# Performance work log

Hardware: AMD Instinct MI355X
Metric: run time of the kernel (lower is better)

Reference implementation:

```python
import jax, jax.numpy as jnp
import numpy as np
from jax import lax

S, T, B = 32, 32, 512          # src len, tgt len, batch
H, E, A = 1024, 256, 1024      # hidden, embed, attention dim
VS, VT = 64, 70                # source / target char vocab
START = 1                      # data.tar_l2i[start_token]


def _gru_cell(gi, h, W_hh, b_hh):
    """torch GRUCell math. gi = x @ W_ih.T + b_ih, shape (B, 3H)."""
    gh = h @ W_hh.T + b_hh
    ir, iz, in_ = jnp.split(gi, 3, axis=-1)
    hr, hz, hn = jnp.split(gh, 3, axis=-1)
    r = jax.nn.sigmoid(ir + hr)
    z = jax.nn.sigmoid(iz + hz)
    n = jnp.tanh(in_ + r * hn)
    return (1.0 - z) * n + z * h


def setup_inputs() -> dict:
    key = jax.random.key(0)
    ks = jax.random.split(key, 16)
    n = lambda k, shp: jax.random.normal(k, shp, dtype=jnp.float32) * 0.05
    return {
        "source": jax.random.randint(ks[0], (S, B), 0, VS),
        "target": jax.random.randint(ks[1], (T, B), 0, VT),
        "teacher_forcing": 1,
        "emb_src": n(ks[2], (VS, E)),
        "W_ih_enc": n(ks[3], (3 * H, E)),
        "W_hh_enc": n(ks[4], (3 * H, H)),
        "b_ih_enc": n(ks[5], (3 * H,)),
        "b_hh_enc": n(ks[6], (3 * H,)),
        "emb_tgt": n(ks[7], (VT, E)),
        "W_attn": n(ks[8], (2 * H, A)),
        "b_attn": n(ks[9], (A,)),
        "v_attn": n(ks[10], (A,)),
        "W_ih_dec": n(ks[11], (3 * H, H + E)),
        "W_hh_dec": n(ks[12], (3 * H, H)),
        "b_ih_dec": n(ks[13], (3 * H,)),
        "b_hh_dec": n(ks[14], (3 * H,)),
        "W_out": n(ks[15], (H, VT)),
        "b_out": jnp.zeros((VT,), jnp.float32),
    }


def reference(source, target, teacher_forcing, emb_src, W_ih_enc, W_hh_enc,
              b_ih_enc, b_hh_enc, emb_tgt, W_attn, b_attn, v_attn,
              W_ih_dec, W_hh_dec, b_ih_dec, b_hh_dec, W_out, b_out):
    tf = bool(teacher_forcing)

    # ---------------- Encoder: GRU over (S, B) ----------------
    x_emb = emb_src[source]                                   # (S, B, E)
    # precompute input-to-hidden GEMM for all timesteps (big fused GEMM)
    gi_all = jnp.einsum('sbe,ge->sbg', x_emb, W_ih_enc) + b_ih_enc  # (S, B, 3H)

    def enc_step(h, gi_t):
        h = _gru_cell(gi_t, h, W_hh_enc, b_hh_enc)
        return h, h

    h0 = jnp.zeros((B, H), x_emb.dtype)
    h_enc, enc_ops = lax.scan(enc_step, h0, gi_all)           # enc_ops: (S, B, H)

    # ---------------- Decoder loop (t = 1 .. T-1) ----------------
    def dec_step(carry, tgt_t):
        h, x = carry
        emb = emb_tgt[x]                                      # (B, E)
        hx = jnp.broadcast_to(h[None], (S, B, H))
        feat = jnp.concatenate([hx, enc_ops], axis=-1)        # (S, B, 2H)
        energy = jnp.tanh(jnp.einsum('sbf,fa->sba', feat, W_attn) + b_attn)
        scores = energy @ v_attn                              # (S, B)
        alpha = jax.nn.softmax(scores, axis=0)                # over source positions
        ctx = jnp.einsum('sb,sbh->bh', alpha, enc_ops)        # (B, H)
        gi = jnp.concatenate([ctx, emb], axis=-1) @ W_ih_dec.T + b_ih_dec
        h_new = _gru_cell(gi, h, W_hh_dec, b_hh_dec)
        logits = h_new @ W_out + b_out                        # (B, VT)
        x_next = tgt_t if tf else jnp.argmax(logits, axis=1)
        return (h_new, x_next), (logits, alpha.T)             # attn row: (B, S)

    (_, _), (dec_logits, attn) = lax.scan(dec_step, (h_enc, target[0]), target[1:])

    # outputs[0] is the one-hot start token (outputs[:, :, start]=1, rows 1.. overwritten)
    row0 = jnp.zeros((B, VT), dec_logits.dtype).at[:, START].set(1.0)
    outputs = jnp.concatenate([row0[None], dec_logits], axis=0)  # (T, B, VT)
    return outputs, attn                                         # attn: (T-1, B, S)
```

## Files before the change

kernel.cpp:

```cpp
#include <hip/hip_runtime.h>
#include <hip/hip_bf16.h>

typedef __bf16 bfx8 __attribute__((ext_vector_type(8)));
typedef __bf16 bfx4 __attribute__((ext_vector_type(4)));
typedef float f32x4 __attribute__((ext_vector_type(4)));

#define MFMA __builtin_amdgcn_mfma_f32_16x16x32_bf16


__device__ __attribute__((aligned(256))) float  g_h[512 * 1024];
__device__ __attribute__((aligned(256))) float  g_hpart[512 * 1024];
__device__ __attribute__((aligned(256))) __bf16 g_hb[2][512 * 1024];
__device__ __attribute__((aligned(256))) __bf16 g_Adec[512 * 1280];
__device__ __attribute__((aligned(256))) __bf16 g_enc_ops[(size_t)32 * 512 * 1024];
__device__ __attribute__((aligned(256))) __bf16 g_enc_part[(size_t)32 * 512 * 1024];
__device__ __attribute__((aligned(256))) __bf16 g_sWhhe[(size_t)3072 * 1024];
__device__ __attribute__((aligned(256))) __bf16 g_sWihe[(size_t)3072 * 256];
__device__ __attribute__((aligned(256))) __bf16 g_sWhhd[(size_t)3072 * 1024];
__device__ __attribute__((aligned(256))) __bf16 g_sWihd[(size_t)3072 * 1280];
__device__ __attribute__((aligned(256))) __bf16 g_sWattnA[(size_t)1024 * 1024];
__device__ __attribute__((aligned(256))) __bf16 g_sWattnB[(size_t)1024 * 1024];
__device__ __attribute__((aligned(256))) __bf16 g_sWout[(size_t)128 * 1024];
__device__ __attribute__((aligned(256))) __bf16 g_embs[64 * 256];
__device__ __attribute__((aligned(256))) __bf16 g_embt[70 * 256];

__device__ __forceinline__ float fast_tanh(float x) {
    float cx = fminf(fmaxf(x, -15.f), 15.f);
    float e = __expf(-2.f * cx);
    return (1.f - e) / (1.f + e);
}

__global__ void k_cvt(const float* __restrict__ src, __bf16* __restrict__ dst,
                      int n4)
{
    int i = blockIdx.x * 256 + threadIdx.x;
    if (i >= n4) return;
    float4 v = ((const float4*)src)[i];
    __bf16 o[4] = {(__bf16)v.x, (__bf16)v.y, (__bf16)v.z, (__bf16)v.w};
    *(ushort2*)(dst + 4 * i) = *(ushort2*)o;
    *(ushort2*)(dst + 4 * i + 2) = *(ushort2*)(o + 2);
}

__global__ void swz_rm(const float* __restrict__ W, __bf16* __restrict__ out,
                       int nK, int total)
{
    int gid = blockIdx.x * 256 + threadIdx.x;
    if (gid >= total) return;
    int F = gid >> 6, L = gid & 63;
    int t = F / nK, c = F - t * nK;
    int K = nK * 32;
    const float* s = W + (size_t)(t * 16 + (L & 15)) * K + c * 32 + (L >> 4) * 8;
    __bf16 o[8];
#pragma unroll
    for (int u = 0; u < 8; u++) o[u] = (__bf16)s[u];
    *(uint4*)(out + (size_t)gid * 8) = *(uint4*)o;
}

__global__ void swz_cm(const float* __restrict__ W, __bf16* __restrict__ out,
                       int nK, int ldsrc, int nguard, int total)
{
    int gid = blockIdx.x * 256 + threadIdx.x;
    if (gid >= total) return;
    int F = gid >> 6, L = gid & 63;
    int t = F / nK, c = F - t * nK;
    int n = t * 16 + (L & 15);
    int k = c * 32 + (L >> 4) * 8;
    __bf16 o[8];
#pragma unroll
    for (int u = 0; u < 8; u++)
        o[u] = (n < nguard) ? (__bf16)W[(size_t)(k + u) * ldsrc + n] : (__bf16)0.f;
    *(uint4*)(out + (size_t)gid * 8) = *(uint4*)o;
}

__global__ void k_init(float* __restrict__ out)
{
    int idx = blockIdx.x * 256 + threadIdx.x;
    if (idx < 512 * 1024) { g_h[idx] = 0.f; g_hb[0][idx] = (__bf16)0.f; }
    if (idx < 512 * 70) out[idx] = (idx % 70 == 1) ? 1.f : 0.f;
}

__global__ __launch_bounds__(512, 4) void k_encpart(
    const __bf16* __restrict__ Amat, const __bf16* __restrict__ sW,
    __bf16* __restrict__ Cout)
{
    __shared__ __bf16 sA[2][64 * 256];
    const int tid = threadIdx.x;
    const int w = tid >> 6, lane = tid & 63;
    const int r15 = lane & 15, q = lane >> 4;
    const int n0 = blockIdx.x * 256, m0 = blockIdx.y * 64;

    int sr[4], sv[4], so[4];
#pragma unroll
    for (int i = 0; i < 4; i++) {
        int lin = tid + i * 512;
        sr[i] = lin >> 5;
        sv[i] = lin & 31;
        so[i] = (sr[i] * 32 + (sv[i] ^ (sr[i] & 7))) * 8;
    }

    uint4 regs[4];
#pragma unroll
    for (int i = 0; i < 4; i++)
        regs[i] = *(const uint4*)(Amat + (size_t)(m0 + sr[i]) * 1024 + sv[i] * 8);
#pragma unroll
    for (int i = 0; i < 4; i++)
        *(uint4*)(&sA[0][so[i]]) = regs[i];
    __syncthreads();

    const int xk = r15 & 7;
    f32x4 acc[2][4];
#pragma unroll
    for (int nn = 0; nn < 2; nn++)
#pragma unroll
        for (int mf = 0; mf < 4; mf++) acc[nn][mf] = (f32x4){0.f, 0.f, 0.f, 0.f};

    const __bf16* wp0 = sW + ((size_t)(blockIdx.x * 16 + w * 2) * 32) * 512 + lane * 8;
    const __bf16* wp1 = wp0 + 32 * 512;
    const int ar0 = r15 * 256;
    const int ar1 = (16 + r15) * 256;
    const int ar2 = (32 + r15) * 256;
    const int ar3 = (48 + r15) * 256;

    for (int kc = 0; kc < 4; kc++) {
        if (kc < 3) {
#pragma unroll
            for (int i = 0; i < 4; i++)
                regs[i] = *(const uint4*)(Amat + (size_t)(m0 + sr[i]) * 1024 +
                                          (kc + 1) * 256 + sv[i] * 8);
        }
        const __bf16* sAb = sA[kc & 1];
        const __bf16* wq0 = wp0 + kc * 8 * 512;
        const __bf16* wq1 = wp1 + kc * 8 * 512;
#pragma unroll
        for (int c = 0; c < 8; c++) {
            int us = ((c * 4 + q) ^ xk) * 8;
            bfx8 a0 = *(const bfx8*)(sAb + ar0 + us);
            bfx8 a1 = *(const bfx8*)(sAb + ar1 + us);
            bfx8 a2 = *(const bfx8*)(sAb + ar2 + us);
            bfx8 a3 = *(const bfx8*)(sAb + ar3 + us);
            bfx8 w0 = *(const bfx8*)(wq0 + c * 512);
            bfx8 w1 = *(const bfx8*)(wq1 + c * 512);
            acc[0][0] = MFMA(a0, w0, acc[0][0], 0, 0, 0);
            acc[0][1] = MFMA(a1, w0, acc[0][1], 0, 0, 0);
            acc[0][2] = MFMA(a2, w0, acc[0][2], 0, 0, 0);
            acc[0][3] = MFMA(a3, w0, acc[0][3], 0, 0, 0);
            acc[1][0] = MFMA(a0, w1, acc[1][0], 0, 0, 0);
            acc[1][1] = MFMA(a1, w1, acc[1][1], 0, 0, 0);
            acc[1][2] = MFMA(a2, w1, acc[1][2], 0, 0, 0);
            acc[1][3] = MFMA(a3, w1, acc[1][3], 0, 0, 0);
        }
        if (kc < 3) {
#pragma unroll
            for (int i = 0; i < 4; i++)
                *(uint4*)(&sA[(kc + 1) & 1][so[i]]) = regs[i];
            __syncthreads();
        }
    }

#pragma unroll
    for (int nn = 0; nn < 2; nn++) {
        const int col = n0 + (w * 2 + nn) * 16 + r15;
#pragma unroll
        for (int mf = 0; mf < 4; mf++) {
#pragma unroll
            for (int reg = 0; reg < 4; reg++) {
                int row = m0 + mf * 16 + q * 4 + reg;
                Cout[(size_t)row * 1024 + col] = (__bf16)acc[nn][mf][reg];
            }
        }
    }
}

#define GH_BODY(ACC)                                              \
    {                                                             \
        int us = ((c * 4 + q) ^ xk) * 8;                          \
        bfx8 a0 = *(const bfx8*)(sA1 + br0 + us);                 \
        bfx8 a1 = *(const bfx8*)(sA1 + br1 + us);                 \
        bfx8 w0 = *(const bfx8*)(xp0 + c * 512);                  \
        bfx8 w1 = *(const bfx8*)(xp1 + c * 512);                  \
        bfx8 w2 = *(const bfx8*)(xp2 + c * 512);                  \
        ACC[0][0] = MFMA(a0, w0, ACC[0][0], 0, 0, 0);             \
        ACC[0][1] = MFMA(a1, w0, ACC[0][1], 0, 0, 0);             \
        ACC[1][0] = MFMA(a0, w1, ACC[1][0], 0, 0, 0);             \
        ACC[1][1] = MFMA(a1, w1, ACC[1][1], 0, 0, 0);             \
        ACC[2][0] = MFMA(a0, w2, ACC[2][0], 0, 0, 0);             \
        ACC[2][1] = MFMA(a1, w2, ACC[2][1], 0, 0, 0);             \
    }

__global__ __launch_bounds__(512, 1) void gru_step(
    const __bf16* __restrict__ hb_in, __bf16* __restrict__ hb_out,
    const __bf16* __restrict__ sW1, const float* __restrict__ b1,
    const __bf16* __restrict__ sW2, const float* __restrict__ b2,
    int nK2, const int* __restrict__ src_t, int enc_t)
{
    __shared__ __bf16 sA1[32 * 1024];
    __shared__ __bf16 sA2[32 * 1280];
    const int tid = threadIdx.x;
    const int w = tid >> 6, lane = tid & 63;
    const int r15 = lane & 15, q = lane >> 4;
    const int j0 = blockIdx.x * 64, m0 = blockIdx.y * 32;
    const int jsub = w & 3;

#pragma unroll
    for (int i = 0; i < 8; i++) {
        int lin = tid + i * 512;
        int r = lin >> 7, U = lin & 127;
        uint4 v = *(const uint4*)(hb_in + (size_t)(m0 + r) * 1024 + U * 8);
        *(uint4*)(sA1 + (r * 128 + (U ^ (r & 7))) * 8) = v;
    }
    if (src_t) {
#pragma unroll
        for (int i = 0; i < 2; i++) {
            int lin = tid + i * 512;
            int r = lin >> 5, U = lin & 31;
            int sv = src_t[m0 + r];
            sv = (sv < 0) ? 0 : (sv > 63 ? 63 : sv);
            uint4 v = *(const uint4*)(g_embs + sv * 256 + U * 8);
            *(uint4*)(sA2 + (r * 32 + (U ^ (r & 7))) * 8) = v;
        }
    } else {
        for (int lin = tid; lin < 32 * 160; lin += 512) {
            int r = lin / 160, U = lin - r * 160;
            uint4 v = *(const uint4*)(g_Adec + (size_t)(m0 + r) * 1280 + U * 8);
            *(uint4*)(sA2 + (r * 160 + (U ^ (r & 7))) * 8) = v;
        }
    }
    __syncthreads();

    const size_t tb = (size_t)(blockIdx.x * 4 + jsub);
    const int xk = r15 & 7;
    f32x4 acc[3][2];
#pragma unroll
    for (int s = 0; s < 3; s++)
#pragma unroll
        for (int ms = 0; ms < 2; ms++) acc[s][ms] = (f32x4){0.f, 0.f, 0.f, 0.f};

    if (w < 4) {
        const __bf16* xp0 = sW1 + (tb * 32) * 512 + lane * 8;
        const __bf16* xp1 = sW1 + ((tb + 64) * 32) * 512 + lane * 8;
        const __bf16* xp2 = sW1 + ((tb + 128) * 32) * 512 + lane * 8;
        const int br0 = r15 * 1024, br1 = (16 + r15) * 1024;
        if (src_t) {
#pragma unroll 4
            for (int c = 0; c < 20; c++) GH_BODY(acc)
        } else {
#pragma unroll 8
            for (int c = 0; c < 32; c++) GH_BODY(acc)
        }
    } else {
        const __bf16* wp0 = sW2 + (tb * (size_t)nK2) * 512 + lane * 8;
        const __bf16* wp1 = sW2 + ((tb + 64) * (size_t)nK2) * 512 + lane * 8;
        const __bf16* wp2 = sW2 + ((tb + 128) * (size_t)nK2) * 512 + lane * 8;
        const int ru = nK2 * 4;
        const int gr0 = r15 * ru * 8, gr1 = (16 + r15) * ru * 8;
#pragma unroll 8
        for (int c = 0; c < nK2; c++) {
            int us = ((c * 4 + q) ^ xk) * 8;
            bfx8 a0 = *(const bfx8*)(sA2 + gr0 + us);
            bfx8 a1 = *(const bfx8*)(sA2 + gr1 + us);
            bfx8 w0 = *(const bfx8*)(wp0 + c * 512);
            bfx8 w1 = *(const bfx8*)(wp1 + c * 512);
            bfx8 w2 = *(const bfx8*)(wp2 + c * 512);
            acc[0][0] = MFMA(a0, w0, acc[0][0], 0, 0, 0);
            acc[0][1] = MFMA(a1, w0, acc[0][1], 0, 0, 0);
            acc[1][0] = MFMA(a0, w1, acc[1][0], 0, 0, 0);
            acc[1][1] = MFMA(a1, w1, acc[1][1], 0, 0, 0);
            acc[2][0] = MFMA(a0, w2, acc[2][0], 0, 0, 0);
            acc[2][1] = MFMA(a1, w2, acc[2][1], 0, 0, 0);
        }
        if (src_t) {
            f32x4 acc2[3][2];
#pragma unroll
            for (int s = 0; s < 3; s++)
#pragma unroll
                for (int ms = 0; ms < 2; ms++) acc2[s][ms] = (f32x4){0.f, 0.f, 0.f, 0.f};
            const __bf16* xp0 = sW1 + (tb * 32) * 512 + lane * 8;
            const __bf16* xp1 = sW1 + ((tb + 64) * 32) * 512 + lane * 8;
            const __bf16* xp2 = sW1 + ((tb + 128) * 32) * 512 + lane * 8;
            const int br0 = r15 * 1024, br1 = (16 + r15) * 1024;
#pragma unroll 4
            for (int c = 20; c < 32; c++) GH_BODY(acc2)
            float* sGh = (float*)sA2 + 6144;
#pragma unroll
            for (int s = 0; s < 3; s++)
#pragma unroll
                for (int ms = 0; ms < 2; ms++)
#pragma unroll
                    for (int reg = 0; reg < 4; reg++)
                        sGh[((s * 4 + jsub) * 32 + ms * 16 + q * 4 + reg) * 16 + r15] =
                            acc2[s][ms][reg];
        }
    }
    __syncthreads();
    float* sGi = (float*)sA2;
    if (w >= 4) {
#pragma unroll
        for (int s = 0; s < 3; s++)
#pragma unroll
            for (int ms = 0; ms < 2; ms++)
#pragma unroll
                for (int reg = 0; reg < 4; reg++)
                    sGi[((s * 4 + jsub) * 32 + ms * 16 + q * 4 + reg) * 16 + r15] =
                        acc[s][ms][reg];
    }
    __syncthreads();
    if (w < 4) {
        const int jj = j0 + jsub * 16 + r15;
        const float bb1[3] = {b1[jj], b1[1024 + jj], b1[2048 + jj]};
        const float bb2[3] = {b2[jj], b2[1024 + jj], b2[2048 + jj]};
        const float* sGh = (const float*)sA2 + 6144;
#pragma unroll
        for (int ms = 0; ms < 2; ms++) {
#pragma unroll
            for (int reg = 0; reg < 4; reg++) {
                int bl = ms * 16 + q * 4 + reg;
                int b_ = m0 + bl;
                float e0 = 0.f, e1 = 0.f, e2 = 0.f;
                if (src_t) {
                    e0 = sGh[((0 * 4 + jsub) * 32 + bl) * 16 + r15];
                    e1 = sGh[((1 * 4 + jsub) * 32 + bl) * 16 + r15];
                    e2 = sGh[((2 * 4 + jsub) * 32 + bl) * 16 + r15];
                }
                float gh0 = acc[0][ms][reg] + bb1[0] + e0;
                float gh1 = acc[1][ms][reg] + bb1[1] + e1;
                float gh2 = acc[2][ms][reg] + bb1[2] + e2;
                float gi0 = sGi[((0 * 4 + jsub) * 32 + bl) * 16 + r15] + bb2[0];
                float gi1 = sGi[((1 * 4 + jsub) * 32 + bl) * 16 + r15] + bb2[1];
                float gi2 = sGi[((2 * 4 + jsub) * 32 + bl) * 16 + r15] + bb2[2];
                float r = 1.f / (1.f + __expf(-(gi0 + gh0)));
                float z = 1.f / (1.f + __expf(-(gi1 + gh1)));
                float n = fast_tanh(gi2 + r * gh2);
                size_t off = (size_t)b_ * 1024 + jj;
                float hv = (1.f - z) * n + z * g_h[off];
                g_h[off] = hv;
                hb_out[off] = (__bf16)hv;
                if (enc_t >= 0)
                    g_enc_ops[(size_t)enc_t * 524288 + off] = (__bf16)hv;
            }
        }
    }
}

__global__ __launch_bounds__(256) void k_hl(
    const __bf16* __restrict__ src, const float* __restrict__ battn,
    const float* __restrict__ bout, int lrow, float* __restrict__ outp)
{
    __shared__ __bf16 sA[32 * 1024];
    const int tid = threadIdx.x;
    const int w = tid >> 6, lane = tid & 63;
    const int r15 = lane & 15, q = lane >> 4;
    const int bx = blockIdx.x, m0 = blockIdx.y * 32;

#pragma unroll
    for (int i = 0; i < 16; i++) {
        int lin = tid + i * 256;
        int r = lin >> 7, U = lin & 127;
        uint4 v = *(const uint4*)(src + (size_t)(m0 + r) * 1024 + U * 8);
        *(uint4*)(sA + (r * 128 + (U ^ (r & 7))) * 8) = v;
    }
    __syncthreads();

    const __bf16* sW;
    int n;
    if (bx < 16) {
        sW = g_sWattnA;
        n = bx * 64 + w * 16 + r15;
    } else {
        if (lrow < 0) return;
        sW = g_sWout;
        n = (bx - 16) * 64 + w * 16 + r15;
    }
    const size_t tb = (size_t)((bx < 16 ? bx : bx - 16) * 4 + w);
    const __bf16* wp = sW + (tb * 32) * 512 + lane * 8;
    const int xk = r15 & 7;
    const int ar0 = r15 * 1024, ar1 = (16 + r15) * 1024;

    f32x4 acc[2];
    acc[0] = (f32x4){0.f, 0.f, 0.f, 0.f};
    acc[1] = (f32x4){0.f, 0.f, 0.f, 0.f};
#pragma unroll 8
    for (int c = 0; c < 32; c++) {
        int us = ((c * 4 + q) ^ xk) * 8;
        bfx8 a0 = *(const bfx8*)(sA + ar0 + us);
        bfx8 a1 = *(const bfx8*)(sA + ar1 + us);
        bfx8 wv = *(const bfx8*)(wp + c * 512);
        acc[0] = MFMA(a0, wv, acc[0], 0, 0, 0);
        acc[1] = MFMA(a1, wv, acc[1], 0, 0, 0);
    }

    if (bx < 16) {
        float bv = battn[n];
#pragma unroll
        for (int ms = 0; ms < 2; ms++)
#pragma unroll
            for (int reg = 0; reg < 4; reg++)
                g_hpart[(size_t)(m0 + ms * 16 + q * 4 + reg) * 1024 + n] =
                    acc[ms][reg] + bv;
    } else if (n < 70) {
        float bv = bout[n];
#pragma unroll
        for (int ms = 0; ms < 2; ms++)
#pragma unroll
            for (int reg = 0; reg < 4; reg++)
                outp[(size_t)lrow * 35840 +
                     (size_t)(m0 + ms * 16 + q * 4 + reg) * 70 + n] =
                    acc[ms][reg] + bv;
    }
}

__global__ __launch_bounds__(256) void k_attn(
    int j, const int* __restrict__ target, const int* __restrict__ tf,
    const float* __restrict__ v_attn, float* __restrict__ out)
{
    const int b = blockIdx.x, tid = threadIdx.x;
    const int lane = tid & 63, wave = tid >> 6;
    __shared__ float sc[32], sal[32];
    __shared__ int sx;
    if (wave == 0) {
        int xv;
        if (j == 0) xv = target[b];
        else if (*tf) xv = target[j * 512 + b];
        else {
            const float* row = out + (size_t)j * 35840 + b * 70;
            float bv = row[lane]; int bi = lane;
            if (lane < 6) {
                float v2 = row[lane + 64];
                if (v2 > bv) { bv = v2; bi = lane + 64; }
            }
#pragma unroll
            for (int off = 32; off; off >>= 1) {
                float ov = __shfl_down(bv, off);
                int   oi = __shfl_down(bi, off);
                if (ov > bv || (ov == bv && oi < bi)) { bv = ov; bi = oi; }
            }
            xv = bi;
        }
        if (lane == 0) sx = (xv < 0) ? 0 : (xv > 69 ? 69 : xv);
    }
    float hpv[16], vsv[16];
    {
        const float* hp = g_hpart + (size_t)b * 1024;
#pragma unroll
        for (int u = 0; u < 8; u++) {
            hpv[u]     = hp[lane * 8 + u];
            hpv[8 + u] = hp[512 + lane * 8 + u];
            vsv[u]     = v_attn[lane * 8 + u];
            vsv[8 + u] = v_attn[512 + lane * 8 + u];
        }
    }
    __syncthreads();
    g_Adec[(size_t)b * 1280 + 1024 + tid] = g_embt[sx * 256 + tid];
    for (int s = wave * 8; s < wave * 8 + 8; s++) {
        const __bf16* ep = g_enc_part + ((size_t)s * 512 + b) * 1024;
        bfx8 e0 = *(const bfx8*)(ep + lane * 8);
        bfx8 e1 = *(const bfx8*)(ep + 512 + lane * 8);
        float part = 0.f;
#pragma unroll
        for (int u = 0; u < 8; u++) {
            part += vsv[u]     * fast_tanh((float)e0[u] + hpv[u]);
            part += vsv[8 + u] * fast_tanh((float)e1[u] + hpv[8 + u]);
        }
#pragma unroll
        for (int off = 32; off; off >>= 1) part += __shfl_down(part, off);
        if (lane == 0) sc[s] = part;
    }
    __syncthreads();
    float mx = sc[0];
#pragma unroll
    for (int s = 1; s < 32; s++) mx = fmaxf(mx, sc[s]);
    float den = 0.f;
#pragma unroll
    for (int s = 0; s < 32; s++) den += __expf(sc[s] - mx);
    float rden = 1.f / den;
    if (tid < 32) {
        float al = __expf(sc[tid] - mx) * rden;
        sal[tid] = al;
        out[1146880 + (size_t)j * 16384 + b * 32 + tid] = al;
    }
    __syncthreads();
    float c0 = 0, c1 = 0, c2 = 0, c3 = 0;
    const __bf16* eo = g_enc_ops + (size_t)b * 1024 + tid * 4;
#pragma unroll 4
    for (int s = 0; s < 32; s++) {
        bfx4 e = *(const bfx4*)(eo + (size_t)s * 524288);
        float al = sal[s];
        c0 += al * (float)e[0]; c1 += al * (float)e[1];
        c2 += al * (float)e[2]; c3 += al * (float)e[3];
    }
    bfx4 o = {(__bf16)c0, (__bf16)c1, (__bf16)c2, (__bf16)c3};
    *(bfx4*)(&g_Adec[(size_t)b * 1280 + tid * 4]) = o;
}

extern "C" void kernel_launch(void* const* d_in, const int* in_sizes, int n_in,
                              void* d_out, int out_size, void* d_ws, size_t ws_size,
                              hipStream_t stream)
{
    const int*   source   = (const int*)d_in[0];
    const int*   target   = (const int*)d_in[1];
    const int*   tf       = (const int*)d_in[2];
    const float* emb_src  = (const float*)d_in[3];
    const float* W_ih_enc = (const float*)d_in[4];
    const float* W_hh_enc = (const float*)d_in[5];
    const float* b_ih_enc = (const float*)d_in[6];
    const float* b_hh_enc = (const float*)d_in[7];
    const float* emb_tgt  = (const float*)d_in[8];
    const float* W_attn   = (const float*)d_in[9];
    const float* b_attn   = (const float*)d_in[10];
    const float* v_attn   = (const float*)d_in[11];
    const float* W_ih_dec = (const float*)d_in[12];
    const float* W_hh_dec = (const float*)d_in[13];
    const float* b_ih_dec = (const float*)d_in[14];
    const float* b_hh_dec = (const float*)d_in[15];
    const float* W_out    = (const float*)d_in[16];
    const float* b_out    = (const float*)d_in[17];
    float* out = (float*)d_out;

    void *p_hb, *p_sWhhe, *p_sWihe, *p_sWhhd, *p_sWihd, *p_sWattnA, *p_sWattnB,
         *p_sWout, *p_embs, *p_embt, *p_enc_ops, *p_enc_part;
    hipGetSymbolAddress(&p_hb,       HIP_SYMBOL(g_hb));
    hipGetSymbolAddress(&p_sWhhe,    HIP_SYMBOL(g_sWhhe));
    hipGetSymbolAddress(&p_sWihe,    HIP_SYMBOL(g_sWihe));
    hipGetSymbolAddress(&p_sWhhd,    HIP_SYMBOL(g_sWhhd));
    hipGetSymbolAddress(&p_sWihd,    HIP_SYMBOL(g_sWihd));
    hipGetSymbolAddress(&p_sWattnA,  HIP_SYMBOL(g_sWattnA));
    hipGetSymbolAddress(&p_sWattnB,  HIP_SYMBOL(g_sWattnB));
    hipGetSymbolAddress(&p_sWout,    HIP_SYMBOL(g_sWout));
    hipGetSymbolAddress(&p_embs,     HIP_SYMBOL(g_embs));
    hipGetSymbolAddress(&p_embt,     HIP_SYMBOL(g_embt));
    hipGetSymbolAddress(&p_enc_ops,  HIP_SYMBOL(g_enc_ops));
    hipGetSymbolAddress(&p_enc_part, HIP_SYMBOL(g_enc_part));
    __bf16* hb0 = (__bf16*)p_hb;
    __bf16* hb1 = hb0 + 512 * 1024;

    k_cvt<<<16, 256, 0, stream>>>(emb_src, (__bf16*)p_embs, 64 * 256 / 4);
    k_cvt<<<18, 256, 0, stream>>>(emb_tgt, (__bf16*)p_embt, 70 * 256 / 4);
    swz_rm<<<1536, 256, 0, stream>>>(W_hh_enc, (__bf16*)p_sWhhe, 32, 393216);
    swz_rm<<<384,  256, 0, stream>>>(W_ih_enc, (__bf16*)p_sWihe, 8,  98304);
    swz_rm<<<1536, 256, 0, stream>>>(W_hh_dec, (__bf16*)p_sWhhd, 32, 393216);
    swz_rm<<<1920, 256, 0, stream>>>(W_ih_dec, (__bf16*)p_sWihd, 40, 491520);
    swz_cm<<<512,  256, 0, stream>>>(W_attn, (__bf16*)p_sWattnA, 32, 1024, 1024, 131072);
    swz_cm<<<512,  256, 0, stream>>>(W_attn + (size_t)1024 * 1024,
                                     (__bf16*)p_sWattnB, 32, 1024, 1024, 131072);
    swz_cm<<<64,   256, 0, stream>>>(W_out,  (__bf16*)p_sWout,   32, 70,   70,   16384);
    k_init<<<2048, 256, 0, stream>>>(out);

    for (int t = 0; t < 32; t++) {
        __bf16* hin  = (t & 1) ? hb1 : hb0;
        __bf16* hout = (t & 1) ? hb0 : hb1;
        gru_step<<<dim3(16, 16), 512, 0, stream>>>(
            hin, hout, (__bf16*)p_sWhhe, b_hh_enc,
            (__bf16*)p_sWihe, b_ih_enc, 8, source + t * 512, t);
    }

    k_encpart<<<dim3(4, 256), 512, 0, stream>>>(
        (__bf16*)p_enc_ops, (__bf16*)p_sWattnB, (__bf16*)p_enc_part);

    k_hl<<<dim3(18, 16), 256, 0, stream>>>(hb0, b_attn, b_out, -1, out);

    for (int j = 0; j < 31; j++) {
        __bf16* hin  = (j & 1) ? hb1 : hb0;
        __bf16* hout = (j & 1) ? hb0 : hb1;
        k_attn<<<512, 256, 0, stream>>>(j, target, tf, v_attn, out);
        gru_step<<<dim3(16, 16), 512, 0, stream>>>(
            hin, hout, (__bf16*)p_sWhhd, b_hh_dec,
            (__bf16*)p_sWihd, b_ih_dec, 40, nullptr, -1);
        k_hl<<<dim3(18, 16), 256, 0, stream>>>(hout, b_attn, b_out, j + 1, out);
    }
}
```

Baseline: 2.550 ms.

## Fuse encoder and decoder step loops into persistent cooperative kernels with grid sync

Replaces the per-timestep kernel launches (32 encoder GRU steps, and 31×3 decoder attention/GRU/projection launches) with two persistent cooperative kernels of 256 blocks that loop over timesteps and separate phases with grid-wide barriers. The attention and projection phases are remapped so that each 512-thread block handles two 256-thread sub-tasks, sharing one large dynamic-style shared buffer. The encoder-projection GEMM grid is flattened and swizzled so that neighbouring blocks reuse weight tiles. The aim is to remove launch overhead and inter-kernel gaps, at the cost of grid.sync latency, a requirement that all 256 blocks be co-resident (one per CU), and shared-memory sizing that limits occupancy.

```diff
diff --git a/kernel.cpp b/kernel.cpp
--- a/kernel.cpp
+++ b/kernel.cpp
@@ -1,5 +1,8 @@
 #include <hip/hip_runtime.h>
 #include <hip/hip_bf16.h>
+#include <hip/hip_cooperative_groups.h>
+
+namespace cg = cooperative_groups;
 
 typedef __bf16 bfx8 __attribute__((ext_vector_type(8)));
 typedef __bf16 bfx4 __attribute__((ext_vector_type(4)));
@@ -87,7 +90,9 @@
     const int tid = threadIdx.x;
     const int w = tid >> 6, lane = tid & 63;
     const int r15 = lane & 15, q = lane >> 4;
-    const int n0 = blockIdx.x * 256, m0 = blockIdx.y * 64;
+    const int sw = (blockIdx.x & 7) * 128 + (blockIdx.x >> 3);
+    const int nx = sw & 3;
+    const int n0 = nx * 256, m0 = (sw >> 2) * 64;
 
     int sr[4], sv[4], so[4];
 #pragma unroll
@@ -114,7 +119,7 @@
 #pragma unroll
         for (int mf = 0; mf < 4; mf++) acc[nn][mf] = (f32x4){0.f, 0.f, 0.f, 0.f};
 
-    const __bf16* wp0 = sW + ((size_t)(blockIdx.x * 16 + w * 2) * 32) * 512 + lane * 8;
+    const __bf16* wp0 = sW + ((size_t)(nx * 16 + w * 2) * 32) * 512 + lane * 8;
     const __bf16* wp1 = wp0 + 32 * 512;
     const int ar0 = r15 * 256;
     const int ar1 = (16 + r15) * 256;
@@ -187,18 +192,18 @@
         ACC[2][1] = MFMA(a1, w2, ACC[2][1], 0, 0, 0);             \
     }
 
-__global__ __launch_bounds__(512, 1) void gru_step(
-    const __bf16* __restrict__ hb_in, __bf16* __restrict__ hb_out,
-    const __bf16* __restrict__ sW1, const float* __restrict__ b1,
-    const __bf16* __restrict__ sW2, const float* __restrict__ b2,
-    int nK2, const int* __restrict__ src_t, int enc_t)
-{
-    __shared__ __bf16 sA1[32 * 1024];
-    __shared__ __bf16 sA2[32 * 1280];
+__device__ __forceinline__ void gru_phase(
+    unsigned char* smem_, const __bf16* hb_in, __bf16* hb_out,
+    const __bf16* sW1, const float* b1,
+    const __bf16* sW2, const float* b2,
+    int nK2, const int* src_t, int enc_t, int bid)
+{
+    __bf16* sA1 = (__bf16*)smem_;
+    __bf16* sA2 = (__bf16*)(smem_ + 65536);
     const int tid = threadIdx.x;
     const int w = tid >> 6, lane = tid & 63;
     const int r15 = lane & 15, q = lane >> 4;
-    const int j0 = blockIdx.x * 64, m0 = blockIdx.y * 32;
+    const int j0 = (bid & 15) * 64, m0 = (bid >> 4) * 32;
     const int jsub = w & 3;
 
 #pragma unroll
@@ -227,7 +232,7 @@
     }
     __syncthreads();
 
-    const size_t tb = (size_t)(blockIdx.x * 4 + jsub);
+    const size_t tb = (size_t)((bid & 15) * 4 + jsub);
     const int xk = r15 & 7;
     f32x4 acc[3][2];
 #pragma unroll
@@ -341,24 +346,32 @@
     }
 }
 
-__global__ __launch_bounds__(256) void k_hl(
-    const __bf16* __restrict__ src, const float* __restrict__ battn,
-    const float* __restrict__ bout, int lrow, float* __restrict__ outp)
-{
-    __shared__ __bf16 sA[32 * 1024];
+__device__ __forceinline__ void hl_phase(
+    unsigned char* smem_, const __bf16* src, const float* battn,
+    const float* bout, int lrow, float* outp, int bid)
+{
     const int tid = threadIdx.x;
-    const int w = tid >> 6, lane = tid & 63;
+    const int half = tid >> 8, t2 = tid & 255;
+    __bf16* sA = (__bf16*)(smem_ + half * 65536);
+    const int vb = bid + 256 * half;
+    const int active = vb < 288;
+    int bx = 0, m0 = 0;
+    if (active) { bx = vb % 18; m0 = (vb / 18) * 32; }
+    const int w = t2 >> 6, lane = tid & 63;
     const int r15 = lane & 15, q = lane >> 4;
-    const int bx = blockIdx.x, m0 = blockIdx.y * 32;
-
-#pragma unroll
-    for (int i = 0; i < 16; i++) {
-        int lin = tid + i * 256;
-        int r = lin >> 7, U = lin & 127;
-        uint4 v = *(const uint4*)(src + (size_t)(m0 + r) * 1024 + U * 8);
-        *(uint4*)(sA + (r * 128 + (U ^ (r & 7))) * 8) = v;
-    }
-    __syncthreads();
+    const int comp = active && !(bx >= 16 && lrow < 0);
+
+    if (comp) {
+#pragma unroll
+        for (int i = 0; i < 16; i++) {
+            int lin = t2 + i * 256;
+            int r = lin >> 7, U = lin & 127;
+            uint4 v = *(const uint4*)(src + (size_t)(m0 + r) * 1024 + U * 8);
+            *(uint4*)(sA + (r * 128 + (U ^ (r & 7))) * 8) = v;
+        }
+    }
+    __syncthreads();
+    if (!comp) return;
 
     const __bf16* sW;
     int n;
@@ -366,7 +379,6 @@
         sW = g_sWattnA;
         n = bx * 64 + w * 16 + r15;
     } else {
-        if (lrow < 0) return;
         sW = g_sWout;
         n = (bx - 16) * 64 + w * 16 + r15;
     }
@@ -408,15 +420,19 @@
     }
 }
 
-__global__ __launch_bounds__(256) void k_attn(
-    int j, const int* __restrict__ target, const int* __restrict__ tf,
-    const float* __restrict__ v_attn, float* __restrict__ out)
-{
-    const int b = blockIdx.x, tid = threadIdx.x;
-    const int lane = tid & 63, wave = tid >> 6;
-    __shared__ float sc[32], sal[32];
-    __shared__ int sx;
-    if (wave == 0) {
+__device__ __forceinline__ void attn_phase(
+    unsigned char* smem_, int j, const int* target, const int* tf,
+    const float* v_attn, float* out, int bid)
+{
+    const int tid = threadIdx.x;
+    const int half = tid >> 8, t2 = tid & 255;
+    const int b = bid * 2 + half;
+    const int lane = tid & 63, wave2 = t2 >> 6;
+    float* scH  = (float*)smem_ + half * 32;
+    float* salH = (float*)smem_ + 64 + half * 32;
+    int*   sxH  = (int*)(smem_ + 512) + half;
+
+    if (wave2 == 0) {
         int xv;
         if (j == 0) xv = target[b];
         else if (*tf) xv = target[j * 512 + b];
@@ -435,7 +451,7 @@
             }
             xv = bi;
         }
-        if (lane == 0) sx = (xv < 0) ? 0 : (xv > 69 ? 69 : xv);
+        if (lane == 0) *sxH = (xv < 0) ? 0 : (xv > 69 ? 69 : xv);
     }
     float hpv[16], vsv[16];
     {
@@ -449,8 +465,9 @@
         }
     }
     __syncthreads();
-    g_Adec[(size_t)b * 1280 + 1024 + tid] = g_embt[sx * 256 + tid];
-    for (int s = wave * 8; s < wave * 8 + 8; s++) {
+    int sx = *sxH;
+    g_Adec[(size_t)b * 1280 + 1024 + t2] = g_embt[sx * 256 + t2];
+    for (int s = wave2 * 8; s < wave2 * 8 + 8; s++) {
         const __bf16* ep = g_enc_part + ((size_t)s * 512 + b) * 1024;
         bfx8 e0 = *(const bfx8*)(ep + lane * 8);
         bfx8 e1 = *(const bfx8*)(ep + 512 + lane * 8);
@@ -462,33 +479,78 @@
         }
 #pragma unroll
         for (int off = 32; off; off >>= 1) part += __shfl_down(part, off);
-        if (lane == 0) sc[s] = part;
-    }
-    __syncthreads();
-    float mx = sc[0];
-#pragma unroll
-    for (int s = 1; s < 32; s++) mx = fmaxf(mx, sc[s]);
+        if (lane == 0) scH[s] = part;
+    }
+    __syncthreads();
+    float mx = scH[0];
+#pragma unroll
+    for (int s = 1; s < 32; s++) mx = fmaxf(mx, scH[s]);
     float den = 0.f;
 #pragma unroll
-    for (int s = 0; s < 32; s++) den += __expf(sc[s] - mx);
+    for (int s = 0; s < 32; s++) den += __expf(scH[s] - mx);
     float rden = 1.f / den;
-    if (tid < 32) {
-        float al = __expf(sc[tid] - mx) * rden;
-        sal[tid] = al;
-        out[1146880 + (size_t)j * 16384 + b * 32 + tid] = al;
+    if (t2 < 32) {
+        float al = __expf(scH[t2] - mx) * rden;
+        salH[t2] = al;
+        out[1146880 + (size_t)j * 16384 + b * 32 + t2] = al;
     }
     __syncthreads();
     float c0 = 0, c1 = 0, c2 = 0, c3 = 0;
-    const __bf16* eo = g_enc_ops + (size_t)b * 1024 + tid * 4;
+    const __bf16* eo = g_enc_ops + (size_t)b * 1024 + t2 * 4;
 #pragma unroll 4
     for (int s = 0; s < 32; s++) {
         bfx4 e = *(const bfx4*)(eo + (size_t)s * 524288);
-        float al = sal[s];
+        float al = salH[s];
         c0 += al * (float)e[0]; c1 += al * (float)e[1];
         c2 += al * (float)e[2]; c3 += al * (float)e[3];
     }
     bfx4 o = {(__bf16)c0, (__bf16)c1, (__bf16)c2, (__bf16)c3};
-    *(bfx4*)(&g_Adec[(size_t)b * 1280 + tid * 4]) = o;
+    *(bfx4*)(&g_Adec[(size_t)b * 1280 + t2 * 4]) = o;
+}
+
+__global__ void __launch_bounds__(512, 1) enc_all(
+    const int* __restrict__ source, const float* __restrict__ b1,
+    const float* __restrict__ b2, __bf16* __restrict__ hb0,
+    __bf16* __restrict__ hb1)
+{
+    __shared__ __align__(16) unsigned char smem[147456];
+    cg::grid_group grid = cg::this_grid();
+    const int bid = blockIdx.x;
+    __bf16* ha = hb0;
+    __bf16* hb = hb1;
+    for (int t = 0; t < 32; t++) {
+        if (t) grid.sync();
+        gru_phase(smem, ha, hb, g_sWhhe, b1, g_sWihe, b2, 8,
+                  source + t * 512, t, bid);
+        __bf16* tmp = ha; ha = hb; hb = tmp;
+    }
+}
+
+__global__ void __launch_bounds__(512, 1) dec_all(
+    const int* __restrict__ target, const int* __restrict__ tf,
+    const float* __restrict__ v_attn, const float* __restrict__ battn,
+    const float* __restrict__ bout, const float* __restrict__ b1,
+    const float* __restrict__ b2, float* __restrict__ out,
+    __bf16* __restrict__ hb0, __bf16* __restrict__ hb1)
+{
+    __shared__ __align__(16) unsigned char smem[147456];
+    cg::grid_group grid = cg::this_grid();
+    const int bid = blockIdx.x;
+
+    hl_phase(smem, hb0, battn, bout, -1, out, bid);
+    grid.sync();
+
+    __bf16* ha = hb0;
+    __bf16* hb = hb1;
+    for (int j = 0; j < 31; j++) {
+        attn_phase(smem, j, target, tf, v_attn, out, bid);
+        grid.sync();
+        gru_phase(smem, ha, hb, g_sWhhd, b1, g_sWihd, b2, 40, nullptr, -1, bid);
+        grid.sync();
+        hl_phase(smem, hb, battn, bout, j + 1, out, bid);
+        if (j < 30) grid.sync();
+        __bf16* tmp = ha; ha = hb; hb = tmp;
+    }
 }
 
 extern "C" void kernel_launch(void* const* d_in, const int* in_sizes, int n_in,
@@ -544,26 +606,21 @@
     swz_cm<<<64,   256, 0, stream>>>(W_out,  (__bf16*)p_sWout,   32, 70,   70,   16384);
     k_init<<<2048, 256, 0, stream>>>(out);
 
-    for (int t = 0; t < 32; t++) {
-        __bf16* hin  = (t & 1) ? hb1 : hb0;
-        __bf16* hout = (t & 1) ? hb0 : hb1;
-        gru_step<<<dim3(16, 16), 512, 0, stream>>>(
-            hin, hout, (__bf16*)p_sWhhe, b_hh_enc,
-            (__bf16*)p_sWihe, b_ih_enc, 8, source + t * 512, t);
-    }
-
-    k_encpart<<<dim3(4, 256), 512, 0, stream>>>(
+    {
+        void* args[] = {(void*)&source, (void*)&b_hh_enc, (void*)&b_ih_enc,
+                        (void*)&hb0, (void*)&hb1};
+        hipLaunchCooperativeKernel((const void*)enc_all, dim3(256), dim3(512),
+                                   args, 0, stream);
+    }
+
+    k_encpart<<<dim3(1024), 512, 0, stream>>>(
         (__bf16*)p_enc_ops, (__bf16*)p_sWattnB, (__bf16*)p_enc_part);
 
-    k_hl<<<dim3(18, 16), 256, 0, stream>>>(hb0, b_attn, b_out, -1, out);
-
-    for (int j = 0; j < 31; j++) {
-        __bf16* hin  = (j & 1) ? hb1 : hb0;
-        __bf16* hout = (j & 1) ? hb0 : hb1;
-        k_attn<<<512, 256, 0, stream>>>(j, target, tf, v_attn, out);
-        gru_step<<<dim3(16, 16), 512, 0, stream>>>(
-            hin, hout, (__bf16*)p_sWhhd, b_hh_dec,
-            (__bf16*)p_sWihd, b_ih_dec, 40, nullptr, -1);
-        k_hl<<<dim3(18, 16), 256, 0, stream>>>(hout, b_attn, b_out, j + 1, out);
-    }
-}
+    {
+        void* args[] = {(void*)&target, (void*)&tf, (void*)&v_attn,
+                        (void*)&b_attn, (void*)&b_out, (void*)&b_hh_dec,
+                        (void*)&b_ih_dec, (void*)&out, (void*)&hb0, (void*)&hb1};
+        hipLaunchCooperativeKernel((const void*)dec_all, dim3(256), dim3(512),
+                                   args, 0, stream);
+    }
+}
```

Result: slower. 6.755 ms (+164.9%).

## Split GRU step into smaller 256-thread blocks and remap encoder-part grid

Applied to the files above, without the earlier changes.

The GRU step kernel now runs 256-thread blocks covering 32 hidden columns each, with twice as many blocks and two blocks allowed per CU, to raise occupancy. The input-side operands (embeddings or the decoder input row) are read straight from global memory instead of being staged in shared memory, and the work is rebalanced so the hidden-side waves also take a slice of the decoder input GEMM. The encoder-part GEMM grid is flattened and remapped with a swizzled block order to improve cache locality. Reading operands directly from global memory trades shared-memory reuse for fewer barriers and less LDS use, and may cost extra global traffic.

```diff
diff --git a/kernel.cpp b/kernel.cpp
--- a/kernel.cpp
+++ b/kernel.cpp
@@ -87,7 +87,9 @@
     const int tid = threadIdx.x;
     const int w = tid >> 6, lane = tid & 63;
     const int r15 = lane & 15, q = lane >> 4;
-    const int n0 = blockIdx.x * 256, m0 = blockIdx.y * 64;
+    const int sw = (blockIdx.x & 7) * 128 + (blockIdx.x >> 3);
+    const int nx = sw & 3;
+    const int n0 = nx * 256, m0 = (sw >> 2) * 64;
 
     int sr[4], sv[4], so[4];
 #pragma unroll
@@ -114,7 +116,7 @@
 #pragma unroll
         for (int mf = 0; mf < 4; mf++) acc[nn][mf] = (f32x4){0.f, 0.f, 0.f, 0.f};
 
-    const __bf16* wp0 = sW + ((size_t)(blockIdx.x * 16 + w * 2) * 32) * 512 + lane * 8;
+    const __bf16* wp0 = sW + ((size_t)(nx * 16 + w * 2) * 32) * 512 + lane * 8;
     const __bf16* wp1 = wp0 + 32 * 512;
     const int ar0 = r15 * 256;
     const int ar1 = (16 + r15) * 256;
@@ -187,55 +189,58 @@
         ACC[2][1] = MFMA(a1, w2, ACC[2][1], 0, 0, 0);             \
     }
 
-__global__ __launch_bounds__(512, 1) void gru_step(
+#define GI_BODY(ACC)                                              \
+    {                                                             \
+        bfx8 a0 = *(const bfx8*)(A0 + c * 32);                    \
+        bfx8 a1 = *(const bfx8*)(A1 + c * 32);                    \
+        bfx8 w0 = *(const bfx8*)(wp0 + c * 512);                  \
+        bfx8 w1 = *(const bfx8*)(wp1 + c * 512);                  \
+        bfx8 w2 = *(const bfx8*)(wp2 + c * 512);                  \
+        ACC[0][0] = MFMA(a0, w0, ACC[0][0], 0, 0, 0);             \
+        ACC[0][1] = MFMA(a1, w0, ACC[0][1], 0, 0, 0);             \
+        ACC[1][0] = MFMA(a0, w1, ACC[1][0], 0, 0, 0);             \
+        ACC[1][1] = MFMA(a1, w1, ACC[1][1], 0, 0, 0);             \
+        ACC[2][0] = MFMA(a0, w2, ACC[2][0], 0, 0, 0);             \
+        ACC[2][1] = MFMA(a1, w2, ACC[2][1], 0, 0, 0);             \
+    }
+
+__global__ __launch_bounds__(256, 2) void gru_step(
     const __bf16* __restrict__ hb_in, __bf16* __restrict__ hb_out,
     const __bf16* __restrict__ sW1, const float* __restrict__ b1,
     const __bf16* __restrict__ sW2, const float* __restrict__ b2,
     int nK2, const int* __restrict__ src_t, int enc_t)
 {
-    __shared__ __bf16 sA1[32 * 1024];
-    __shared__ __bf16 sA2[32 * 1280];
+    __shared__ __align__(16) unsigned char smem[77824];
+    __bf16* sA1 = (__bf16*)smem;
+    float*  sGi = (float*)smem;
+    float*  sGh = (float*)(smem + 65536);
     const int tid = threadIdx.x;
     const int w = tid >> 6, lane = tid & 63;
     const int r15 = lane & 15, q = lane >> 4;
-    const int j0 = blockIdx.x * 64, m0 = blockIdx.y * 32;
-    const int jsub = w & 3;
-
-#pragma unroll
-    for (int i = 0; i < 8; i++) {
-        int lin = tid + i * 512;
+    const int j0 = blockIdx.x * 32, m0 = blockIdx.y * 32;
+    const int jsub = w & 1;
+
+#pragma unroll
+    for (int i = 0; i < 16; i++) {
+        int lin = tid + i * 256;
         int r = lin >> 7, U = lin & 127;
         uint4 v = *(const uint4*)(hb_in + (size_t)(m0 + r) * 1024 + U * 8);
         *(uint4*)(sA1 + (r * 128 + (U ^ (r & 7))) * 8) = v;
     }
-    if (src_t) {
-#pragma unroll
-        for (int i = 0; i < 2; i++) {
-            int lin = tid + i * 512;
-            int r = lin >> 5, U = lin & 31;
-            int sv = src_t[m0 + r];
-            sv = (sv < 0) ? 0 : (sv > 63 ? 63 : sv);
-            uint4 v = *(const uint4*)(g_embs + sv * 256 + U * 8);
-            *(uint4*)(sA2 + (r * 32 + (U ^ (r & 7))) * 8) = v;
-        }
-    } else {
-        for (int lin = tid; lin < 32 * 160; lin += 512) {
-            int r = lin / 160, U = lin - r * 160;
-            uint4 v = *(const uint4*)(g_Adec + (size_t)(m0 + r) * 1280 + U * 8);
-            *(uint4*)(sA2 + (r * 160 + (U ^ (r & 7))) * 8) = v;
-        }
-    }
-    __syncthreads();
-
-    const size_t tb = (size_t)(blockIdx.x * 4 + jsub);
+    __syncthreads();
+
+    const size_t tb = (size_t)(blockIdx.x * 2 + jsub);
     const int xk = r15 & 7;
-    f32x4 acc[3][2];
+    f32x4 acc[3][2], acc2[3][2];
 #pragma unroll
     for (int s = 0; s < 3; s++)
 #pragma unroll
-        for (int ms = 0; ms < 2; ms++) acc[s][ms] = (f32x4){0.f, 0.f, 0.f, 0.f};
-
-    if (w < 4) {
+        for (int ms = 0; ms < 2; ms++) {
+            acc[s][ms]  = (f32x4){0.f, 0.f, 0.f, 0.f};
+            acc2[s][ms] = (f32x4){0.f, 0.f, 0.f, 0.f};
+        }
+
+    if (w < 2) {
         const __bf16* xp0 = sW1 + (tb * 32) * 512 + lane * 8;
         const __bf16* xp1 = sW1 + ((tb + 64) * 32) * 512 + lane * 8;
         const __bf16* xp2 = sW1 + ((tb + 128) * 32) * 512 + lane * 8;
@@ -246,87 +251,86 @@
         } else {
 #pragma unroll 8
             for (int c = 0; c < 32; c++) GH_BODY(acc)
+            const __bf16* wp0 = sW2 + (tb * 40) * 512 + lane * 8;
+            const __bf16* wp1 = sW2 + ((tb + 64) * 40) * 512 + lane * 8;
+            const __bf16* wp2 = sW2 + ((tb + 128) * 40) * 512 + lane * 8;
+            const __bf16* A0 = g_Adec + (size_t)(m0 + r15) * 1280 + q * 8;
+            const __bf16* A1 = A0 + 16 * 1280;
+#pragma unroll
+            for (int c = 36; c < 40; c++) GI_BODY(acc2)
         }
     } else {
-        const __bf16* wp0 = sW2 + (tb * (size_t)nK2) * 512 + lane * 8;
-        const __bf16* wp1 = sW2 + ((tb + 64) * (size_t)nK2) * 512 + lane * 8;
-        const __bf16* wp2 = sW2 + ((tb + 128) * (size_t)nK2) * 512 + lane * 8;
-        const int ru = nK2 * 4;
-        const int gr0 = r15 * ru * 8, gr1 = (16 + r15) * ru * 8;
-#pragma unroll 8
-        for (int c = 0; c < nK2; c++) {
-            int us = ((c * 4 + q) ^ xk) * 8;
-            bfx8 a0 = *(const bfx8*)(sA2 + gr0 + us);
-            bfx8 a1 = *(const bfx8*)(sA2 + gr1 + us);
-            bfx8 w0 = *(const bfx8*)(wp0 + c * 512);
-            bfx8 w1 = *(const bfx8*)(wp1 + c * 512);
-            bfx8 w2 = *(const bfx8*)(wp2 + c * 512);
-            acc[0][0] = MFMA(a0, w0, acc[0][0], 0, 0, 0);
-            acc[0][1] = MFMA(a1, w0, acc[0][1], 0, 0, 0);
-            acc[1][0] = MFMA(a0, w1, acc[1][0], 0, 0, 0);
-            acc[1][1] = MFMA(a1, w1, acc[1][1], 0, 0, 0);
-            acc[2][0] = MFMA(a0, w2, acc[2][0], 0, 0, 0);
-            acc[2][1] = MFMA(a1, w2, acc[2][1], 0, 0, 0);
-        }
         if (src_t) {
-            f32x4 acc2[3][2];
-#pragma unroll
-            for (int s = 0; s < 3; s++)
-#pragma unroll
-                for (int ms = 0; ms < 2; ms++) acc2[s][ms] = (f32x4){0.f, 0.f, 0.f, 0.f};
+            int s0 = src_t[m0 + r15];      s0 = (s0 < 0) ? 0 : (s0 > 63 ? 63 : s0);
+            int s1 = src_t[m0 + 16 + r15]; s1 = (s1 < 0) ? 0 : (s1 > 63 ? 63 : s1);
+            const __bf16* A0 = g_embs + s0 * 256 + q * 8;
+            const __bf16* A1 = g_embs + s1 * 256 + q * 8;
+            const __bf16* wp0 = sW2 + (tb * 8) * 512 + lane * 8;
+            const __bf16* wp1 = sW2 + ((tb + 64) * 8) * 512 + lane * 8;
+            const __bf16* wp2 = sW2 + ((tb + 128) * 8) * 512 + lane * 8;
+#pragma unroll
+            for (int c = 0; c < 8; c++) GI_BODY(acc)
             const __bf16* xp0 = sW1 + (tb * 32) * 512 + lane * 8;
             const __bf16* xp1 = sW1 + ((tb + 64) * 32) * 512 + lane * 8;
             const __bf16* xp2 = sW1 + ((tb + 128) * 32) * 512 + lane * 8;
             const int br0 = r15 * 1024, br1 = (16 + r15) * 1024;
 #pragma unroll 4
             for (int c = 20; c < 32; c++) GH_BODY(acc2)
-            float* sGh = (float*)sA2 + 6144;
 #pragma unroll
             for (int s = 0; s < 3; s++)
 #pragma unroll
                 for (int ms = 0; ms < 2; ms++)
 #pragma unroll
                     for (int reg = 0; reg < 4; reg++)
-                        sGh[((s * 4 + jsub) * 32 + ms * 16 + q * 4 + reg) * 16 + r15] =
+                        sGh[((s * 2 + jsub) * 32 + ms * 16 + q * 4 + reg) * 16 + r15] =
                             acc2[s][ms][reg];
-        }
-    }
-    __syncthreads();
-    float* sGi = (float*)sA2;
-    if (w >= 4) {
+        } else {
+            const __bf16* A0 = g_Adec + (size_t)(m0 + r15) * 1280 + q * 8;
+            const __bf16* A1 = A0 + 16 * 1280;
+            const __bf16* wp0 = sW2 + (tb * 40) * 512 + lane * 8;
+            const __bf16* wp1 = sW2 + ((tb + 64) * 40) * 512 + lane * 8;
+            const __bf16* wp2 = sW2 + ((tb + 128) * 40) * 512 + lane * 8;
+#pragma unroll 4
+            for (int c = 0; c < 36; c++) GI_BODY(acc)
+        }
+    }
+    __syncthreads();
+    if (w >= 2) {
 #pragma unroll
         for (int s = 0; s < 3; s++)
 #pragma unroll
             for (int ms = 0; ms < 2; ms++)
 #pragma unroll
                 for (int reg = 0; reg < 4; reg++)
-                    sGi[((s * 4 + jsub) * 32 + ms * 16 + q * 4 + reg) * 16 + r15] =
+                    sGi[((s * 2 + jsub) * 32 + ms * 16 + q * 4 + reg) * 16 + r15] =
                         acc[s][ms][reg];
     }
     __syncthreads();
-    if (w < 4) {
+    if (w < 2) {
         const int jj = j0 + jsub * 16 + r15;
         const float bb1[3] = {b1[jj], b1[1024 + jj], b1[2048 + jj]};
         const float bb2[3] = {b2[jj], b2[1024 + jj], b2[2048 + jj]};
-        const float* sGh = (const float*)sA2 + 6144;
 #pragma unroll
         for (int ms = 0; ms < 2; ms++) {
 #pragma unroll
             for (int reg = 0; reg < 4; reg++) {
                 int bl = ms * 16 + q * 4 + reg;
                 int b_ = m0 + bl;
-                float e0 = 0.f, e1 = 0.f, e2 = 0.f;
+                float gh0 = acc[0][ms][reg] + bb1[0];
+                float gh1 = acc[1][ms][reg] + bb1[1];
+                float gh2 = acc[2][ms][reg] + bb1[2];
+                float gi0 = sGi[((0 * 2 + jsub) * 32 + bl) * 16 + r15] + bb2[0];
+                float gi1 = sGi[((1 * 2 + jsub) * 32 + bl) * 16 + r15] + bb2[1];
+                float gi2 = sGi[((2 * 2 + jsub) * 32 + bl) * 16 + r15] + bb2[2];
                 if (src_t) {
-                    e0 = sGh[((0 * 4 + jsub) * 32 + bl) * 16 + r15];
-                    e1 = sGh[((1 * 4 + jsub) * 32 + bl) * 16 + r15];
-                    e2 = sGh[((2 * 4 + jsub) * 32 + bl) * 16 + r15];
+                    gh0 += sGh[((0 * 2 + jsub) * 32 + bl) * 16 + r15];
+                    gh1 += sGh[((1 * 2 + jsub) * 32 + bl) * 16 + r15];
+                    gh2 += sGh[((2 * 2 + jsub) * 32 + bl) * 16 + r15];
+                } else {
+                    gi0 += acc2[0][ms][reg];
+                    gi1 += acc2[1][ms][reg];
+                    gi2 += acc2[2][ms][reg];
                 }
-                float gh0 = acc[0][ms][reg] + bb1[0] + e0;
-                float gh1 = acc[1][ms][reg] + bb1[1] + e1;
-                float gh2 = acc[2][ms][reg] + bb1[2] + e2;
-                float gi0 = sGi[((0 * 4 + jsub) * 32 + bl) * 16 + r15] + bb2[0];
-                float gi1 = sGi[((1 * 4 + jsub) * 32 + bl) * 16 + r15] + bb2[1];
-                float gi2 = sGi[((2 * 4 + jsub) * 32 + bl) * 16 + r15] + bb2[2];
                 float r = 1.f / (1.f + __expf(-(gi0 + gh0)));
                 float z = 1.f / (1.f + __expf(-(gi1 + gh1)));
                 float n = fast_tanh(gi2 + r * gh2);
@@ -547,12 +551,12 @@
     for (int t = 0; t < 32; t++) {
         __bf16* hin  = (t & 1) ? hb1 : hb0;
         __bf16* hout = (t & 1) ? hb0 : hb1;
-        gru_step<<<dim3(16, 16), 512, 0, stream>>>(
+        gru_step<<<dim3(32, 16), 256, 0, stream>>>(
             hin, hout, (__bf16*)p_sWhhe, b_hh_enc,
             (__bf16*)p_sWihe, b_ih_enc, 8, source + t * 512, t);
     }
 
-    k_encpart<<<dim3(4, 256), 512, 0, stream>>>(
+    k_encpart<<<dim3(1024), 512, 0, stream>>>(
         (__bf16*)p_enc_ops, (__bf16*)p_sWattnB, (__bf16*)p_enc_part);
 
     k_hl<<<dim3(18, 16), 256, 0, stream>>>(hb0, b_attn, b_out, -1, out);
@@ -561,7 +565,7 @@
         __bf16* hin  = (j & 1) ? hb1 : hb0;
         __bf16* hout = (j & 1) ? hb0 : hb1;
         k_attn<<<512, 256, 0, stream>>>(j, target, tf, v_attn, out);
-        gru_step<<<dim3(16, 16), 512, 0, stream>>>(
+        gru_step<<<dim3(32, 16), 256, 0, stream>>>(
             hin, hout, (__bf16*)p_sWhhd, b_hh_dec,
             (__bf16*)p_sWihd, b_ih_dec, 40, nullptr, -1);
         k_hl<<<dim3(18, 16), 256, 0, stream>>>(hout, b_attn, b_out, j + 1, out);
```

Measured after the change: 2.275 ms. -10.8%, faster.
